# Kernel tuning notes

Hardware: AMD Instinct MI355X
Metric: run time of the kernel (lower is better)

## Reference

```python
import jax, jax.numpy as jnp
import numpy as np

D_MODEL = 256
N_HEAD = 4
HEAD_DIM = D_MODEL // N_HEAD  # 64


def setup_inputs() -> dict:
    key = jax.random.key(0)
    kx, kw, kb = jax.random.split(key, 3)
    x = jax.random.normal(kx, (4, 2048, D_MODEL), dtype=jnp.float32)
    # nn.Linear(256, 768): weight [768, 256], bias [768]
    bound = 1.0 / np.sqrt(D_MODEL)
    W_qkv = jax.random.uniform(kw, (3 * D_MODEL, D_MODEL), dtype=jnp.float32, minval=-bound, maxval=bound)
    b_qkv = jax.random.uniform(kb, (3 * D_MODEL,), dtype=jnp.float32, minval=-bound, maxval=bound)
    return {"x": x, "W_qkv": W_qkv, "b_qkv": b_qkv}


def reference(x, W_qkv, b_qkv):
    B, S, _ = x.shape
    # fused QKV projection: [B, S, 3*D]
    qkv = jnp.einsum("bsd,ed->bse", x, W_qkv) + b_qkv
    q, k, v = jnp.split(qkv, 3, axis=-1)
    # [B, S, D] -> [B, H, S, Dh]
    def to_heads(t):
        return t.reshape(B, S, N_HEAD, HEAD_DIM).transpose(0, 2, 1, 3)
    q, k, v = to_heads(q), to_heads(k), to_heads(v)
    scale = 1.0 / np.sqrt(HEAD_DIM)
    # scores [B, H, S, S]
    scores = jnp.einsum("bhqd,bhkd->bhqk", q, k) * scale
    attn = jax.nn.softmax(scores, axis=-1)
    out = jnp.einsum("bhqk,bhkd->bhqd", attn, v)  # [B, H, S, Dh]
    return out
```

## Files before the change

kernel.cpp:

```cpp
#include <hip/hip_runtime.h>

#define BB 4
#define SS 2048
#define DM 256
#define NH 4
#define DH 64
#define NROW (BB*SS)
#define NE   (3*DM)
#define BH   (BB*NH)
#define HEAD_ELEMS (BH*SS*DH)
#define NQROWS (BH*SS)

typedef _Float16 half_t;
typedef __attribute__((ext_vector_type(8))) _Float16 half8;
typedef __attribute__((ext_vector_type(4))) _Float16 half4;
typedef __attribute__((ext_vector_type(4))) float floatx4;

#define KPAD 72

#define QK_SCALE 0.18033688011112042f
#define EXP2(x) __builtin_amdgcn_exp2f(x)
#define DEFER_THR 8.0f

__global__ __launch_bounds__(256) void prep(const float* __restrict__ x,
                                            const float* __restrict__ W,
                                            half_t* __restrict__ xh,
                                            half_t* __restrict__ xl,
                                            half_t* __restrict__ wh) {
    int gtid = blockIdx.x * 256 + threadIdx.x;
    {
        int i = gtid * 4;
        float4 v = *(const float4*)&x[i];
        half4 h, l;
        h.x = (half_t)v.x; l.x = (half_t)(v.x - (float)h.x);
        h.y = (half_t)v.y; l.y = (half_t)(v.y - (float)h.y);
        h.z = (half_t)v.z; l.z = (half_t)(v.z - (float)h.z);
        h.w = (half_t)v.w; l.w = (half_t)(v.w - (float)h.w);
        *(half4*)&xh[i] = h;
        *(half4*)&xl[i] = l;
    }
    if (gtid < NE * DM / 4) {
        int i = gtid * 4;
        float4 v = *(const float4*)&W[i];
        half4 h;
        h.x = (half_t)v.x; h.y = (half_t)v.y;
        h.z = (half_t)v.z; h.w = (half_t)v.w;
        *(half4*)&wh[i] = h;
    }
}

__global__ __launch_bounds__(256) void qkv_proj(const half_t* __restrict__ xh,
                                                const half_t* __restrict__ xl,
                                                const half_t* __restrict__ whg,
                                                const float* __restrict__ bias,
                                                half_t* __restrict__ qh,
                                                half_t* __restrict__ kh,
                                                half_t* __restrict__ vt) {
    __shared__ __align__(16) half_t Xh[64 * KPAD];
    __shared__ __align__(16) half_t Xl[64 * KPAD];
    __shared__ __align__(16) half_t Wh[64 * KPAD];

    const int rb   = blockIdx.x * 64;
    const int nb   = blockIdx.y * 64;
    const int tid  = threadIdx.x;
    const int wid  = tid >> 6;
    const int lane = tid & 63;
    const int quad = lane >> 4;
    const int col  = lane & 15;

    floatx4 acc[4];
    #pragma unroll
    for (int t = 0; t < 4; ++t) acc[t] = (floatx4){0.f, 0.f, 0.f, 0.f};

    for (int k0 = 0; k0 < DM; k0 += 64) {
        __syncthreads();
        #pragma unroll
        for (int i = 0; i < 2; ++i) {
            int gi = tid + 256 * i;
            int r  = gi >> 3;
            int c8 = (gi & 7) * 8;
            *(half8*)&Xh[r * KPAD + c8] = *(const half8*)&xh[(size_t)(rb + r) * DM + k0 + c8];
            *(half8*)&Xl[r * KPAD + c8] = *(const half8*)&xl[(size_t)(rb + r) * DM + k0 + c8];
            *(half8*)&Wh[r * KPAD + c8] = *(const half8*)&whg[(size_t)(nb + r) * DM + k0 + c8];
        }
        __syncthreads();

        half8 ah0 = *(const half8*)&Xh[(wid * 16 + col) * KPAD + quad * 8];
        half8 ah1 = *(const half8*)&Xh[(wid * 16 + col) * KPAD + 32 + quad * 8];
        half8 al0 = *(const half8*)&Xl[(wid * 16 + col) * KPAD + quad * 8];
        half8 al1 = *(const half8*)&Xl[(wid * 16 + col) * KPAD + 32 + quad * 8];

        #pragma unroll
        for (int t = 0; t < 4; ++t) {
            half8 bh0 = *(const half8*)&Wh[(t * 16 + col) * KPAD + quad * 8];
            half8 bh1 = *(const half8*)&Wh[(t * 16 + col) * KPAD + 32 + quad * 8];
            acc[t] = __builtin_amdgcn_mfma_f32_16x16x32_f16(ah0, bh0, acc[t], 0, 0, 0);
            acc[t] = __builtin_amdgcn_mfma_f32_16x16x32_f16(ah1, bh1, acc[t], 0, 0, 0);
            acc[t] = __builtin_amdgcn_mfma_f32_16x16x32_f16(al0, bh0, acc[t], 0, 0, 0);
            acc[t] = __builtin_amdgcn_mfma_f32_16x16x32_f16(al1, bh1, acc[t], 0, 0, 0);
        }
    }

    const int part = nb >> 8;
    const int mloc = wid * 16 + quad * 4;
    if (part != 2) {
        #pragma unroll
        for (int t = 0; t < 4; ++t) {
            int e    = nb + t * 16 + col;
            float be = bias[e];
            int dm   = e & 255;
            int h    = dm >> 6;
            int dh   = dm & 63;
            #pragma unroll
            for (int r = 0; r < 4; ++r) {
                int row = rb + mloc + r;
                int b   = row >> 11;
                int s   = row & 2047;
                int bh_ = b * NH + h;
                float val = acc[t][r] + be;
                if (part == 0) {
                    qh[((size_t)bh_ * SS + s) * DH + dh] = (half_t)(val * QK_SCALE);
                } else {
                    kh[((size_t)bh_ * SS + s) * DH + dh] = (half_t)val;
                }
            }
        }
    } else {
        __syncthreads();
        #pragma unroll
        for (int t = 0; t < 4; ++t) {
            int e    = nb + t * 16 + col;
            float be = bias[e];
            #pragma unroll
            for (int r = 0; r < 4; ++r)
                Xh[(t * 16 + col) * KPAD + mloc + r] = (half_t)(acc[t][r] + be);
        }
        __syncthreads();
        const int b   = rb >> 11;
        const int s0  = rb & 2047;
        const int h   = (nb >> 6) & 3;
        const int bh_ = b * NH + h;
        #pragma unroll
        for (int i = 0; i < 2; ++i) {
            int idx = tid + 256 * i;
            int rr  = idx >> 3;
            int cc8 = (idx & 7) * 8;
            *(half8*)&vt[((size_t)bh_ * DH + rr) * SS + s0 + cc8] =
                *(const half8*)&Xh[rr * KPAD + cc8];
        }
    }
}

__global__ __launch_bounds__(256, 4) void attn(const half_t* __restrict__ qh,
                                               const half_t* __restrict__ kh,
                                               const half_t* __restrict__ vt,
                                               half_t* __restrict__ pO,
                                               float* __restrict__ mst,
                                               float* __restrict__ lst) {
    __shared__ __align__(16) half_t Ks[64 * KPAD];
    __shared__ __align__(16) half_t Vts[64 * KPAD];

    const int q0   = blockIdx.x * 64;
    const int bh   = blockIdx.y;
    const int kz   = blockIdx.z;
    const size_t base = (size_t)bh * SS * DH;
    const int tid  = threadIdx.x;
    const int wid  = tid >> 6;
    const int lane = tid & 63;
    const int quad = lane >> 4;
    const int col  = lane & 15;
    const int ktBeg = kz * (SS / 2);
    const int ktEnd = ktBeg + (SS / 2);

    int srr[2], scc[2];
    #pragma unroll
    for (int i = 0; i < 2; ++i) {
        int gi = tid + 256 * i;
        srr[i] = gi >> 3;
        scc[i] = (gi & 7) * 8;
    }

    half8 bq0, bq1;
    {
        int s = q0 + wid * 16 + col;
        bq0 = *(const half8*)&qh[base + (size_t)s * DH + quad * 8];
        bq1 = *(const half8*)&qh[base + (size_t)s * DH + 32 + quad * 8];
    }

    half8 ck[2], cv[2], nk[2], nv[2];
    #pragma unroll
    for (int i = 0; i < 2; ++i) {
        ck[i] = *(const half8*)&kh[base + (size_t)(ktBeg + srr[i]) * DH + scc[i]];
        cv[i] = *(const half8*)&vt[base + (size_t)srr[i] * SS + ktBeg + scc[i]];
        nk[i] = ck[i];
        nv[i] = cv[i];
    }

    float m_i = -3.0e38f;
    float l_i = 0.f;
    floatx4 o[4];
    #pragma unroll
    for (int dt = 0; dt < 4; ++dt) o[dt] = (floatx4){0.f, 0.f, 0.f, 0.f};

    for (int kt = ktBeg; kt < ktEnd; kt += 64) {
        __syncthreads();
        #pragma unroll
        for (int i = 0; i < 2; ++i) {
            *(half8*)&Ks[srr[i] * KPAD + scc[i]]  = ck[i];
            *(half8*)&Vts[srr[i] * KPAD + scc[i]] = cv[i];
        }
        __syncthreads();

        const int ktn = kt + 64;
        if (ktn < ktEnd) {
            #pragma unroll
            for (int i = 0; i < 2; ++i) {
                nk[i] = *(const half8*)&kh[base + (size_t)(ktn + srr[i]) * DH + scc[i]];
                nv[i] = *(const half8*)&vt[base + (size_t)srr[i] * SS + ktn + scc[i]];
            }
        }

        floatx4 sc[4];
        #pragma unroll
        for (int t = 0; t < 4; ++t) {
            half8 ak0 = *(const half8*)&Ks[(t * 16 + col) * KPAD + quad * 8];
            half8 ak1 = *(const half8*)&Ks[(t * 16 + col) * KPAD + 32 + quad * 8];
            floatx4 c = (floatx4){0.f, 0.f, 0.f, 0.f};
            c = __builtin_amdgcn_mfma_f32_16x16x32_f16(ak0, bq0, c, 0, 0, 0);
            c = __builtin_amdgcn_mfma_f32_16x16x32_f16(ak1, bq1, c, 0, 0, 0);
            sc[t] = c;
        }

        float mloc = -3.0e38f;
        #pragma unroll
        for (int t = 0; t < 4; ++t) {
            float a = fmaxf(fmaxf(sc[t][0], sc[t][1]), fmaxf(sc[t][2], sc[t][3]));
            mloc = fmaxf(mloc, a);
        }
        mloc = fmaxf(mloc, __shfl_xor(mloc, 16));
        mloc = fmaxf(mloc, __shfl_xor(mloc, 32));

        bool skip = __all(mloc <= m_i + DEFER_THR);
        float m_new = skip ? m_i : fmaxf(m_i, mloc);

        half4 pa[4];
        float rsum = 0.f;
        #pragma unroll
        for (int t = 0; t < 4; ++t) {
            float p0 = EXP2(sc[t][0] - m_new);
            float p1 = EXP2(sc[t][1] - m_new);
            float p2 = EXP2(sc[t][2] - m_new);
            float p3 = EXP2(sc[t][3] - m_new);
            rsum += p0 + p1 + p2 + p3;
            pa[t] = (half4){(half_t)p0, (half_t)p1, (half_t)p2, (half_t)p3};
        }
        rsum += __shfl_xor(rsum, 16);
        rsum += __shfl_xor(rsum, 32);

        if (skip) {
            l_i += rsum;
        } else {
            float alpha = EXP2(m_i - m_new);
            m_i = m_new;
            l_i = l_i * alpha + rsum;
            float ar[4];
            #pragma unroll
            for (int i = 0; i < 4; ++i) ar[i] = __shfl(alpha, quad * 4 + i);
            #pragma unroll
            for (int dt = 0; dt < 4; ++dt)
                #pragma unroll
                for (int i = 0; i < 4; ++i)
                    o[dt][i] *= ar[i];
        }

        #pragma unroll
        for (int t = 0; t < 4; ++t) {
            #pragma unroll
            for (int dt = 0; dt < 4; ++dt) {
                half4 bv = *(const half4*)&Vts[(dt * 16 + col) * KPAD + t * 16 + quad * 4];
                o[dt] = __builtin_amdgcn_mfma_f32_16x16x16f16(pa[t], bv, o[dt], 0, 0, 0);
            }
        }

        #pragma unroll
        for (int i = 0; i < 2; ++i) { ck[i] = nk[i]; cv[i] = nv[i]; }
    }

    const size_t pbase = (size_t)kz * HEAD_ELEMS + base;
    {
        float inv = 1.0f / l_i;
        float ir[4];
        #pragma unroll
        for (int i = 0; i < 4; ++i) ir[i] = __shfl(inv, quad * 4 + i);
        #pragma unroll
        for (int dt = 0; dt < 4; ++dt)
            #pragma unroll
            for (int i = 0; i < 4; ++i) {
                int row = q0 + wid * 16 + quad * 4 + i;
                pO[pbase + (size_t)row * DH + dt * 16 + col] = (half_t)(o[dt][i] * ir[i]);
            }
        if (quad == 0) {
            int row = q0 + wid * 16 + col;
            int idx = kz * NQROWS + bh * SS + row;
            mst[idx] = m_i;
            lst[idx] = l_i;
        }
    }
}

__global__ __launch_bounds__(256) void merge(const half_t* __restrict__ pO,
                                             const float* __restrict__ mst,
                                             const float* __restrict__ lst,
                                             float* __restrict__ out) {
    int gid = blockIdx.x * 256 + threadIdx.x;
    int row = gid >> 3;
    int dc  = (gid & 7) * 8;
    float m1 = mst[row], m2 = mst[NQROWS + row];
    float l1 = lst[row], l2 = lst[NQROWS + row];
    float M  = fmaxf(m1, m2);
    float w1 = l1 * EXP2(m1 - M);
    float w2 = l2 * EXP2(m2 - M);
    float inv = 1.0f / (w1 + w2);
    float a = w1 * inv, b = w2 * inv;
    half8 o1 = *(const half8*)&pO[(size_t)row * DH + dc];
    half8 o2 = *(const half8*)&pO[(size_t)HEAD_ELEMS + (size_t)row * DH + dc];
    float4 r0, r1;
    r0.x = a * (float)o1[0] + b * (float)o2[0];
    r0.y = a * (float)o1[1] + b * (float)o2[1];
    r0.z = a * (float)o1[2] + b * (float)o2[2];
    r0.w = a * (float)o1[3] + b * (float)o2[3];
    r1.x = a * (float)o1[4] + b * (float)o2[4];
    r1.y = a * (float)o1[5] + b * (float)o2[5];
    r1.z = a * (float)o1[6] + b * (float)o2[6];
    r1.w = a * (float)o1[7] + b * (float)o2[7];
    *(float4*)&out[(size_t)row * DH + dc]     = r0;
    *(float4*)&out[(size_t)row * DH + dc + 4] = r1;
}

extern "C" void kernel_launch(void* const* d_in, const int* in_sizes, int n_in,
                              void* d_out, int out_size, void* d_ws, size_t ws_size,
                              hipStream_t stream) {
    const float* x  = (const float*)d_in[0];
    const float* Wq = (const float*)d_in[1];
    const float* bq = (const float*)d_in[2];
    float* out = (float*)d_out;

    half_t* qh  = (half_t*)d_ws;
    half_t* kh  = qh + (size_t)HEAD_ELEMS;
    half_t* vt  = kh + (size_t)HEAD_ELEMS;
    half_t* xh  = vt + (size_t)HEAD_ELEMS;
    half_t* xl  = xh + (size_t)HEAD_ELEMS;
    half_t* whp = xl + (size_t)HEAD_ELEMS;
    half_t* pO  = xh;
    float*  mst = (float*)((char*)d_ws + 21364736);
    float*  lst = mst + 2 * NQROWS;

    prep<<<2048, 256, 0, stream>>>(x, Wq, xh, xl, whp);
    qkv_proj<<<dim3(NROW / 64, NE / 64), 256, 0, stream>>>(xh, xl, whp, bq, qh, kh, vt);
    attn<<<dim3(SS / 64, BH, 2), 256, 0, stream>>>(qh, kh, vt, pO, mst, lst);
    merge<<<1024, 256, 0, stream>>>(pO, mst, lst, out);
}
```

Baseline: 118.8 us.

## Double key tile to 128 per iteration and raise wave priority around MFMA

The attention loop now stages 128 keys per iteration instead of 64, with a wider padded V-transpose tile. This halves the number of barrier pairs and softmax reductions per block. The redundant ck/cv register copies are dropped, and s_setprio is raised around the MFMA sections so matrix work gets scheduling priority. In exchange, the kernel uses more LDS and registers (sc and pa double), which may lower occupancy under launch_bounds(256,4).

```diff
diff --git a/kernel.cpp b/kernel.cpp
--- a/kernel.cpp
+++ b/kernel.cpp
@@ -17,6 +17,7 @@
 typedef __attribute__((ext_vector_type(4))) float floatx4;
 
 #define KPAD 72
+#define VPAD 136
 
 #define QK_SCALE 0.18033688011112042f
 #define EXP2(x) __builtin_amdgcn_exp2f(x)
@@ -157,8 +158,8 @@
                                                half_t* __restrict__ pO,
                                                float* __restrict__ mst,
                                                float* __restrict__ lst) {
-    __shared__ __align__(16) half_t Ks[64 * KPAD];
-    __shared__ __align__(16) half_t Vts[64 * KPAD];
+    __shared__ __align__(16) half_t Ks[128 * KPAD];
+    __shared__ __align__(16) half_t Vts[64 * VPAD];
 
     const int q0   = blockIdx.x * 64;
     const int bh   = blockIdx.y;
@@ -172,12 +173,14 @@
     const int ktBeg = kz * (SS / 2);
     const int ktEnd = ktBeg + (SS / 2);
 
-    int srr[2], scc[2];
+    int krr[4], kcc[4], vrr[4], vcc[4];
     #pragma unroll
-    for (int i = 0; i < 2; ++i) {
+    for (int i = 0; i < 4; ++i) {
         int gi = tid + 256 * i;
-        srr[i] = gi >> 3;
-        scc[i] = (gi & 7) * 8;
+        krr[i] = gi >> 3;
+        kcc[i] = (gi & 7) * 8;
+        vrr[i] = gi >> 4;
+        vcc[i] = (gi & 15) * 8;
     }
 
     half8 bq0, bq1;
@@ -187,13 +190,11 @@
         bq1 = *(const half8*)&qh[base + (size_t)s * DH + 32 + quad * 8];
     }
 
-    half8 ck[2], cv[2], nk[2], nv[2];
+    half8 nk[4], nv[4];
     #pragma unroll
-    for (int i = 0; i < 2; ++i) {
-        ck[i] = *(const half8*)&kh[base + (size_t)(ktBeg + srr[i]) * DH + scc[i]];
-        cv[i] = *(const half8*)&vt[base + (size_t)srr[i] * SS + ktBeg + scc[i]];
-        nk[i] = ck[i];
-        nv[i] = cv[i];
+    for (int i = 0; i < 4; ++i) {
+        nk[i] = *(const half8*)&kh[base + (size_t)(ktBeg + krr[i]) * DH + kcc[i]];
+        nv[i] = *(const half8*)&vt[base + (size_t)vrr[i] * SS + ktBeg + vcc[i]];
     }
 
     float m_i = -3.0e38f;
@@ -202,27 +203,28 @@
     #pragma unroll
     for (int dt = 0; dt < 4; ++dt) o[dt] = (floatx4){0.f, 0.f, 0.f, 0.f};
 
-    for (int kt = ktBeg; kt < ktEnd; kt += 64) {
-        __syncthreads();
-        #pragma unroll
-        for (int i = 0; i < 2; ++i) {
-            *(half8*)&Ks[srr[i] * KPAD + scc[i]]  = ck[i];
-            *(half8*)&Vts[srr[i] * KPAD + scc[i]] = cv[i];
-        }
-        __syncthreads();
-
-        const int ktn = kt + 64;
+    for (int kt = ktBeg; kt < ktEnd; kt += 128) {
+        __syncthreads();
+        #pragma unroll
+        for (int i = 0; i < 4; ++i) {
+            *(half8*)&Ks[krr[i] * KPAD + kcc[i]]  = nk[i];
+            *(half8*)&Vts[vrr[i] * VPAD + vcc[i]] = nv[i];
+        }
+        __syncthreads();
+
+        const int ktn = kt + 128;
         if (ktn < ktEnd) {
             #pragma unroll
-            for (int i = 0; i < 2; ++i) {
-                nk[i] = *(const half8*)&kh[base + (size_t)(ktn + srr[i]) * DH + scc[i]];
-                nv[i] = *(const half8*)&vt[base + (size_t)srr[i] * SS + ktn + scc[i]];
+            for (int i = 0; i < 4; ++i) {
+                nk[i] = *(const half8*)&kh[base + (size_t)(ktn + krr[i]) * DH + kcc[i]];
+                nv[i] = *(const half8*)&vt[base + (size_t)vrr[i] * SS + ktn + vcc[i]];
             }
         }
 
-        floatx4 sc[4];
-        #pragma unroll
-        for (int t = 0; t < 4; ++t) {
+        floatx4 sc[8];
+        __builtin_amdgcn_s_setprio(1);
+        #pragma unroll
+        for (int t = 0; t < 8; ++t) {
             half8 ak0 = *(const half8*)&Ks[(t * 16 + col) * KPAD + quad * 8];
             half8 ak1 = *(const half8*)&Ks[(t * 16 + col) * KPAD + 32 + quad * 8];
             floatx4 c = (floatx4){0.f, 0.f, 0.f, 0.f};
@@ -230,10 +232,11 @@
             c = __builtin_amdgcn_mfma_f32_16x16x32_f16(ak1, bq1, c, 0, 0, 0);
             sc[t] = c;
         }
+        __builtin_amdgcn_s_setprio(0);
 
         float mloc = -3.0e38f;
         #pragma unroll
-        for (int t = 0; t < 4; ++t) {
+        for (int t = 0; t < 8; ++t) {
             float a = fmaxf(fmaxf(sc[t][0], sc[t][1]), fmaxf(sc[t][2], sc[t][3]));
             mloc = fmaxf(mloc, a);
         }
@@ -243,10 +246,10 @@
         bool skip = __all(mloc <= m_i + DEFER_THR);
         float m_new = skip ? m_i : fmaxf(m_i, mloc);
 
-        half4 pa[4];
+        half4 pa[8];
         float rsum = 0.f;
         #pragma unroll
-        for (int t = 0; t < 4; ++t) {
+        for (int t = 0; t < 8; ++t) {
             float p0 = EXP2(sc[t][0] - m_new);
             float p1 = EXP2(sc[t][1] - m_new);
             float p2 = EXP2(sc[t][2] - m_new);
@@ -273,17 +276,16 @@
                     o[dt][i] *= ar[i];
         }
 
-        #pragma unroll
-        for (int t = 0; t < 4; ++t) {
+        __builtin_amdgcn_s_setprio(1);
+        #pragma unroll
+        for (int t = 0; t < 8; ++t) {
             #pragma unroll
             for (int dt = 0; dt < 4; ++dt) {
-                half4 bv = *(const half4*)&Vts[(dt * 16 + col) * KPAD + t * 16 + quad * 4];
+                half4 bv = *(const half4*)&Vts[(dt * 16 + col) * VPAD + t * 16 + quad * 4];
                 o[dt] = __builtin_amdgcn_mfma_f32_16x16x16f16(pa[t], bv, o[dt], 0, 0, 0);
             }
         }
-
-        #pragma unroll
-        for (int i = 0; i < 2; ++i) { ck[i] = nk[i]; cv[i] = nv[i]; }
+        __builtin_amdgcn_s_setprio(0);
     }
 
     const size_t pbase = (size_t)kz * HEAD_ELEMS + base;
```

New measurement: 118.7 us. About the same (-0.1%).

## Double-buffer K/V tiles in LDS, software-pipeline PV MFMA, and remap blocks per XCD

Applied to the files above, without the earlier changes.

K and V tiles now go into two LDS buffers with parity switching. The P·V MFMAs of the previous tile are issued right after the current tile's QK^T MFMAs, so the softmax dependency is hidden behind independent matrix work. The prologue zeroes the spare V buffer and P so the first iteration stays correct, and an epilogue finishes the last tile. The block index is also remapped so blocks sharing the same head and key split land on the same XCD, which should improve L2 reuse of K/V. The cost is double the LDS footprint and a longer, more complex loop body.

```diff
diff --git a/kernel.cpp b/kernel.cpp
--- a/kernel.cpp
+++ b/kernel.cpp
@@ -157,12 +157,17 @@
                                                half_t* __restrict__ pO,
                                                float* __restrict__ mst,
                                                float* __restrict__ lst) {
-    __shared__ __align__(16) half_t Ks[64 * KPAD];
-    __shared__ __align__(16) half_t Vts[64 * KPAD];
-
-    const int q0   = blockIdx.x * 64;
-    const int bh   = blockIdx.y;
-    const int kz   = blockIdx.z;
+    __shared__ __align__(16) half_t Ks[2][64 * KPAD];
+    __shared__ __align__(16) half_t Vts[2][64 * KPAD];
+
+    const int lin  = blockIdx.x + 32 * blockIdx.y + 512 * blockIdx.z;
+    const int xcd  = lin & 7;
+    const int j    = lin >> 3;
+    const int strm = xcd + 8 * (j >> 5);
+    const int q0   = (j & 31) * 64;
+    const int bh   = strm & 15;
+    const int kz   = strm >> 4;
+
     const size_t base = (size_t)bh * SS * DH;
     const int tid  = threadIdx.x;
     const int wid  = tid >> 6;
@@ -180,6 +185,12 @@
         scc[i] = (gi & 7) * 8;
     }
 
+    #pragma unroll
+    for (int i = 0; i < 3; ++i) {
+        int idx = tid + 256 * i;
+        if (idx < 576) *(float4*)&Vts[1][idx * 8] = (float4){0.f, 0.f, 0.f, 0.f};
+    }
+
     half8 bq0, bq1;
     {
         int s = q0 + wid * 16 + col;
@@ -187,13 +198,25 @@
         bq1 = *(const half8*)&qh[base + (size_t)s * DH + 32 + quad * 8];
     }
 
-    half8 ck[2], cv[2], nk[2], nv[2];
+    half8 nk[2], nv[2];
     #pragma unroll
     for (int i = 0; i < 2; ++i) {
-        ck[i] = *(const half8*)&kh[base + (size_t)(ktBeg + srr[i]) * DH + scc[i]];
-        cv[i] = *(const half8*)&vt[base + (size_t)srr[i] * SS + ktBeg + scc[i]];
-        nk[i] = ck[i];
-        nv[i] = cv[i];
+        nk[i] = *(const half8*)&kh[base + (size_t)(ktBeg + srr[i]) * DH + scc[i]];
+        nv[i] = *(const half8*)&vt[base + (size_t)srr[i] * SS + ktBeg + scc[i]];
+    }
+    #pragma unroll
+    for (int i = 0; i < 2; ++i) {
+        *(half8*)&Ks[0][srr[i] * KPAD + scc[i]]  = nk[i];
+        *(half8*)&Vts[0][srr[i] * KPAD + scc[i]] = nv[i];
+    }
+    __syncthreads();
+
+    if (ktBeg + 64 < ktEnd) {
+        #pragma unroll
+        for (int i = 0; i < 2; ++i) {
+            nk[i] = *(const half8*)&kh[base + (size_t)(ktBeg + 64 + srr[i]) * DH + scc[i]];
+            nv[i] = *(const half8*)&vt[base + (size_t)srr[i] * SS + ktBeg + 64 + scc[i]];
+        }
     }
 
     float m_i = -3.0e38f;
@@ -201,36 +224,34 @@
     floatx4 o[4];
     #pragma unroll
     for (int dt = 0; dt < 4; ++dt) o[dt] = (floatx4){0.f, 0.f, 0.f, 0.f};
-
+    half4 pa[4];
+    #pragma unroll
+    for (int t = 0; t < 4; ++t) pa[t] = (half4){(half_t)0, (half_t)0, (half_t)0, (half_t)0};
+
+    int parity = 0;
     for (int kt = ktBeg; kt < ktEnd; kt += 64) {
-        __syncthreads();
-        #pragma unroll
-        for (int i = 0; i < 2; ++i) {
-            *(half8*)&Ks[srr[i] * KPAD + scc[i]]  = ck[i];
-            *(half8*)&Vts[srr[i] * KPAD + scc[i]] = cv[i];
-        }
-        __syncthreads();
-
-        const int ktn = kt + 64;
-        if (ktn < ktEnd) {
-            #pragma unroll
-            for (int i = 0; i < 2; ++i) {
-                nk[i] = *(const half8*)&kh[base + (size_t)(ktn + srr[i]) * DH + scc[i]];
-                nv[i] = *(const half8*)&vt[base + (size_t)srr[i] * SS + ktn + scc[i]];
-            }
-        }
+        const int cur = parity, prv = parity ^ 1;
 
         floatx4 sc[4];
         #pragma unroll
         for (int t = 0; t < 4; ++t) {
-            half8 ak0 = *(const half8*)&Ks[(t * 16 + col) * KPAD + quad * 8];
-            half8 ak1 = *(const half8*)&Ks[(t * 16 + col) * KPAD + 32 + quad * 8];
+            half8 ak0 = *(const half8*)&Ks[cur][(t * 16 + col) * KPAD + quad * 8];
+            half8 ak1 = *(const half8*)&Ks[cur][(t * 16 + col) * KPAD + 32 + quad * 8];
             floatx4 c = (floatx4){0.f, 0.f, 0.f, 0.f};
             c = __builtin_amdgcn_mfma_f32_16x16x32_f16(ak0, bq0, c, 0, 0, 0);
             c = __builtin_amdgcn_mfma_f32_16x16x32_f16(ak1, bq1, c, 0, 0, 0);
             sc[t] = c;
         }
 
+        #pragma unroll
+        for (int t = 0; t < 4; ++t) {
+            #pragma unroll
+            for (int dt = 0; dt < 4; ++dt) {
+                half4 bv = *(const half4*)&Vts[prv][(dt * 16 + col) * KPAD + t * 16 + quad * 4];
+                o[dt] = __builtin_amdgcn_mfma_f32_16x16x16f16(pa[t], bv, o[dt], 0, 0, 0);
+            }
+        }
+
         float mloc = -3.0e38f;
         #pragma unroll
         for (int t = 0; t < 4; ++t) {
@@ -243,7 +264,6 @@
         bool skip = __all(mloc <= m_i + DEFER_THR);
         float m_new = skip ? m_i : fmaxf(m_i, mloc);
 
-        half4 pa[4];
         float rsum = 0.f;
         #pragma unroll
         for (int t = 0; t < 4; ++t) {
@@ -273,17 +293,37 @@
                     o[dt][i] *= ar[i];
         }
 
+        __syncthreads();
+        const int ktn = kt + 64;
+        if (ktn < ktEnd) {
+            #pragma unroll
+            for (int i = 0; i < 2; ++i) {
+                *(half8*)&Ks[prv][srr[i] * KPAD + scc[i]]  = nk[i];
+                *(half8*)&Vts[prv][srr[i] * KPAD + scc[i]] = nv[i];
+            }
+            const int ktnn = kt + 128;
+            if (ktnn < ktEnd) {
+                #pragma unroll
+                for (int i = 0; i < 2; ++i) {
+                    nk[i] = *(const half8*)&kh[base + (size_t)(ktnn + srr[i]) * DH + scc[i]];
+                    nv[i] = *(const half8*)&vt[base + (size_t)srr[i] * SS + ktnn + scc[i]];
+                }
+            }
+        }
+        __syncthreads();
+        parity ^= 1;
+    }
+
+    {
+        const int prv = parity ^ 1;
         #pragma unroll
         for (int t = 0; t < 4; ++t) {
             #pragma unroll
             for (int dt = 0; dt < 4; ++dt) {
-                half4 bv = *(const half4*)&Vts[(dt * 16 + col) * KPAD + t * 16 + quad * 4];
+                half4 bv = *(const half4*)&Vts[prv][(dt * 16 + col) * KPAD + t * 16 + quad * 4];
                 o[dt] = __builtin_amdgcn_mfma_f32_16x16x16f16(pa[t], bv, o[dt], 0, 0, 0);
             }
         }
-
-        #pragma unroll
-        for (int i = 0; i < 2; ++i) { ck[i] = nk[i]; cv[i] = nv[i]; }
     }
 
     const size_t pbase = (size_t)kz * HEAD_ELEMS + base;
```

Measured after the change: 120.0 us. No clear change (+1.0%).

## Load V fragments directly from global, double-buffer K in LDS, remap blocks per XCD

Applied to the files above, without the earlier changes.

The attention kernel no longer stages V^T through shared memory. Each lane loads its V fragments for the PV MFMAs straight from global memory into registers at the start of each tile. K moves to a double-buffered LDS tile, which cuts the loop to one barrier per iteration. The block index is also remapped so that blocks sharing the same batch-head and key split land on the same XCD for L2 reuse. The trade-off is more uncoalesced global loads for V (8-byte per lane with an SS stride) and higher register pressure from holding 16 half4 V fragments.

```diff
diff --git a/kernel.cpp b/kernel.cpp
--- a/kernel.cpp
+++ b/kernel.cpp
@@ -157,12 +157,16 @@
                                                half_t* __restrict__ pO,
                                                float* __restrict__ mst,
                                                float* __restrict__ lst) {
-    __shared__ __align__(16) half_t Ks[64 * KPAD];
-    __shared__ __align__(16) half_t Vts[64 * KPAD];
-
-    const int q0   = blockIdx.x * 64;
-    const int bh   = blockIdx.y;
-    const int kz   = blockIdx.z;
+    __shared__ __align__(16) half_t Ks[2][64 * KPAD];
+
+    const int lin  = blockIdx.x + 32 * blockIdx.y + 512 * blockIdx.z;
+    const int xcd  = lin & 7;
+    const int j    = lin >> 3;
+    const int strm = xcd + 8 * (j >> 5);
+    const int q0   = (j & 31) * 64;
+    const int bh   = strm & 15;
+    const int kz   = strm >> 4;
+
     const size_t base = (size_t)bh * SS * DH;
     const int tid  = threadIdx.x;
     const int wid  = tid >> 6;
@@ -187,14 +191,16 @@
         bq1 = *(const half8*)&qh[base + (size_t)s * DH + 32 + quad * 8];
     }
 
-    half8 ck[2], cv[2], nk[2], nv[2];
-    #pragma unroll
-    for (int i = 0; i < 2; ++i) {
-        ck[i] = *(const half8*)&kh[base + (size_t)(ktBeg + srr[i]) * DH + scc[i]];
-        cv[i] = *(const half8*)&vt[base + (size_t)srr[i] * SS + ktBeg + scc[i]];
-        nk[i] = ck[i];
-        nv[i] = cv[i];
-    }
+    const half_t* vcol = vt + base + (size_t)col * SS + quad * 4;
+
+    half8 nk[2];
+    #pragma unroll
+    for (int i = 0; i < 2; ++i)
+        nk[i] = *(const half8*)&kh[base + (size_t)(ktBeg + srr[i]) * DH + scc[i]];
+    #pragma unroll
+    for (int i = 0; i < 2; ++i)
+        *(half8*)&Ks[0][srr[i] * KPAD + scc[i]] = nk[i];
+    __syncthreads();
 
     float m_i = -3.0e38f;
     float l_i = 0.f;
@@ -202,29 +208,28 @@
     #pragma unroll
     for (int dt = 0; dt < 4; ++dt) o[dt] = (floatx4){0.f, 0.f, 0.f, 0.f};
 
+    int parity = 0;
     for (int kt = ktBeg; kt < ktEnd; kt += 64) {
-        __syncthreads();
-        #pragma unroll
-        for (int i = 0; i < 2; ++i) {
-            *(half8*)&Ks[srr[i] * KPAD + scc[i]]  = ck[i];
-            *(half8*)&Vts[srr[i] * KPAD + scc[i]] = cv[i];
-        }
-        __syncthreads();
-
-        const int ktn = kt + 64;
-        if (ktn < ktEnd) {
-            #pragma unroll
-            for (int i = 0; i < 2; ++i) {
-                nk[i] = *(const half8*)&kh[base + (size_t)(ktn + srr[i]) * DH + scc[i]];
-                nv[i] = *(const half8*)&vt[base + (size_t)srr[i] * SS + ktn + scc[i]];
-            }
-        }
+        const int cur = parity, nxt = parity ^ 1;
+
+        half4 bv[4][4];
+        #pragma unroll
+        for (int dt = 0; dt < 4; ++dt)
+            #pragma unroll
+            for (int t = 0; t < 4; ++t)
+                bv[t][dt] = *(const half4*)&vcol[(size_t)(dt * 16) * SS + kt + t * 16];
+
+        int ktn = kt + 64;
+        if (ktn >= ktEnd) ktn = ktBeg;
+        #pragma unroll
+        for (int i = 0; i < 2; ++i)
+            nk[i] = *(const half8*)&kh[base + (size_t)(ktn + srr[i]) * DH + scc[i]];
 
         floatx4 sc[4];
         #pragma unroll
         for (int t = 0; t < 4; ++t) {
-            half8 ak0 = *(const half8*)&Ks[(t * 16 + col) * KPAD + quad * 8];
-            half8 ak1 = *(const half8*)&Ks[(t * 16 + col) * KPAD + 32 + quad * 8];
+            half8 ak0 = *(const half8*)&Ks[cur][(t * 16 + col) * KPAD + quad * 8];
+            half8 ak1 = *(const half8*)&Ks[cur][(t * 16 + col) * KPAD + 32 + quad * 8];
             floatx4 c = (floatx4){0.f, 0.f, 0.f, 0.f};
             c = __builtin_amdgcn_mfma_f32_16x16x32_f16(ak0, bq0, c, 0, 0, 0);
             c = __builtin_amdgcn_mfma_f32_16x16x32_f16(ak1, bq1, c, 0, 0, 0);
@@ -274,16 +279,18 @@
         }
 
         #pragma unroll
-        for (int t = 0; t < 4; ++t) {
-            #pragma unroll
-            for (int dt = 0; dt < 4; ++dt) {
-                half4 bv = *(const half4*)&Vts[(dt * 16 + col) * KPAD + t * 16 + quad * 4];
-                o[dt] = __builtin_amdgcn_mfma_f32_16x16x16f16(pa[t], bv, o[dt], 0, 0, 0);
-            }
-        }
-
-        #pragma unroll
-        for (int i = 0; i < 2; ++i) { ck[i] = nk[i]; cv[i] = nv[i]; }
+        for (int i = 0; i < 2; ++i)
+            *(half8*)&Ks[nxt][srr[i] * KPAD + scc[i]] = nk[i];
+        __syncthreads();
+
+        #pragma unroll
+        for (int t = 0; t < 4; ++t) {
+            #pragma unroll
+            for (int dt = 0; dt < 4; ++dt)
+                o[dt] = __builtin_amdgcn_mfma_f32_16x16x16f16(pa[t], bv[t][dt], o[dt], 0, 0, 0);
+        }
+
+        parity ^= 1;
     }
 
     const size_t pbase = (size_t)kz * HEAD_ELEMS + base;
```

After: 205.6 us. 1.73x slower.
